# Optimization experiments

Hardware: AMD Instinct MI355X
Metric: run time of the kernel (lower is better)

Reference implementation:

```python
import jax, jax.numpy as jnp
import numpy as np

B, N, C = 2, 2048, 2048
H, KV = 16, 4          # query heads, kv heads
D = C // H             # head_dim = 128
ROPE_BASE = 10000.0


def rope_cos_sin(position_ids, dim):
    # interleaved RoPE: freqs for even indices, repeated pairwise to full dim
    inv_freq = 1.0 / (ROPE_BASE ** (jnp.arange(0, dim, 2, dtype=jnp.float32) / dim))
    ang = position_ids[..., None].astype(jnp.float32) * inv_freq   # [B, N, D/2]
    cos = jnp.repeat(jnp.cos(ang), 2, axis=-1)                     # [B, N, D]
    sin = jnp.repeat(jnp.sin(ang), 2, axis=-1)
    return cos, sin


def rotate_half_interleaved(x):
    # (x0, x1, x2, x3, ...) -> (-x1, x0, -x3, x2, ...)
    x1 = x[..., 0::2]
    x2 = x[..., 1::2]
    return jnp.stack([-x2, x1], axis=-1).reshape(x.shape)


def apply_rotary(x, cos, sin):
    # x: [B, h, N, D]; cos/sin: [B, N, D]
    return x * cos[:, None] + rotate_half_interleaved(x) * sin[:, None]


def setup_inputs() -> dict:
    key = jax.random.key(0)
    ks = jax.random.split(key, 5)
    s = 0.02
    return dict(
        x=jax.random.normal(ks[0], (B, N, C), jnp.float32),
        position_ids=jnp.tile(jnp.arange(N, dtype=jnp.int32), (B, 1)),
        Wq=jax.random.normal(ks[1], (C, C), jnp.float32) * s,
        bq=jnp.zeros((C,), jnp.float32),
        Wk=jax.random.normal(ks[2], (C, KV * D), jnp.float32) * s,
        bk=jnp.zeros((KV * D,), jnp.float32),
        Wv=jax.random.normal(ks[3], (C, KV * D), jnp.float32) * s,
        bv=jnp.zeros((KV * D,), jnp.float32),
        Wo=jax.random.normal(ks[4], (C, C), jnp.float32) * s,
    )


def reference(x, position_ids, Wq, bq, Wk, bk, Wv, bv, Wo):
    Bx, Nx, Cx = x.shape
    q = (x @ Wq + bq).reshape(Bx, Nx, H, D).transpose(0, 2, 1, 3)   # [B,H,N,D]
    k = (x @ Wk + bk).reshape(Bx, Nx, KV, D).transpose(0, 2, 1, 3)  # [B,KV,N,D]
    v = (x @ Wv + bv).reshape(Bx, Nx, KV, D).transpose(0, 2, 1, 3)

    cos, sin = rope_cos_sin(position_ids, D)
    q = apply_rotary(q, cos, sin)
    k = apply_rotary(k, cos, sin)

    # GQA expand: head h uses kv head h // groups (matches unsqueeze+expand+reshape)
    groups = H // KV
    k = jnp.repeat(k, groups, axis=1)   # [B,H,N,D]
    v = jnp.repeat(v, groups, axis=1)

    attn = jnp.einsum('bhqd,bhkd->bhqk', q, k) * (D ** -0.5)        # [B,H,N,N]
    causal_mask = jnp.triu(jnp.ones((Nx, Nx), dtype=bool), 1)
    attn = jnp.where(causal_mask, -jnp.inf, attn)
    attn = jax.nn.softmax(attn, axis=-1)

    out = jnp.einsum('bhqk,bhkd->bhqd', attn, v)
    out = out.transpose(0, 2, 1, 3).reshape(Bx, Nx, Cx)
    return out @ Wo
```

## Files before the change

kernel.cpp:

```cpp
#include <hip/hip_runtime.h>
#include <cstdint>
#include <type_traits>

typedef unsigned short u16;
typedef unsigned int u32;
typedef __bf16 bf16x8 __attribute__((ext_vector_type(8)));
typedef float f32x4 __attribute__((ext_vector_type(4)));

constexpr int BB = 2;
constexpr int SEQ = 2048;
constexpr int CH = 2048;
constexpr int NH = 16;
constexpr int NKV = 4;
constexpr int HD = 128;
constexpr int QKVC = CH + 2 * NKV * HD;

#define DI __device__ __forceinline__

DI u16 f2b(float x) {
  u32 u = __float_as_uint(x);
  u = u + 0x7FFFu + ((u >> 16) & 1u);
  return (u16)(u >> 16);
}
DI float b2f(u16 u) { return __uint_as_float(((u32)u) << 16); }

DI u32 pack2bf(float lo, float hi) {
  return __builtin_amdgcn_perm(__float_as_uint(hi), __float_as_uint(lo), 0x07060302u);
}

DI void glds16(const void* g, void* l) {
  __builtin_amdgcn_global_load_lds(
      (__attribute__((address_space(1))) void*)(uintptr_t)g,
      (__attribute__((address_space(3))) void*)(u32)(uintptr_t)l, 16, 0, 0);
}

__global__ __launch_bounds__(256) void prep_kernel(
    const float* __restrict__ x, u16* __restrict__ xb,
    const float* __restrict__ Wq, const float* __restrict__ Wk,
    const float* __restrict__ Wv, const float* __restrict__ Wo,
    u16* __restrict__ wqkvt, u16* __restrict__ wot) {
  if (blockIdx.z == 4) {
    const int n4 = BB * SEQ * CH / 4;
    int base = (blockIdx.x + 32 * blockIdx.y) * 256 + threadIdx.x;
#pragma unroll
    for (int k = 0; k < 8; k++) {
      int i = base + k * 262144;
      if (i < n4) {
        float4 v = *(const float4*)&x[(size_t)i * 4];
        ushort4 o;
        o.x = f2b(v.x); o.y = f2b(v.y); o.z = f2b(v.z); o.w = f2b(v.w);
        *(ushort4*)&xb[(size_t)i * 4] = o;
      }
    }
    return;
  }
  const int z = blockIdx.z;
  const float* in;
  u16* out;
  int Cc;
  if (z == 0)      { in = Wq; out = wqkvt;                                Cc = CH; }
  else if (z == 1) { in = Wk; out = wqkvt + (size_t)CH * CH;              Cc = NKV * HD; }
  else if (z == 2) { in = Wv; out = wqkvt + (size_t)(CH + NKV * HD) * CH; Cc = NKV * HD; }
  else             { in = Wo; out = wot;                                  Cc = CH; }
  if ((int)blockIdx.y * 64 >= Cc) return;

  __shared__ u16 tile[64 * 65];
  const int r0 = blockIdx.x * 64, c0 = blockIdx.y * 64;
  const int tid = threadIdx.x;
  for (int c = tid; c < 1024; c += 256) {
    int r = c >> 4, col = (c & 15) * 4;
    float4 v = *(const float4*)&in[(size_t)(r0 + r) * Cc + c0 + col];
    tile[r * 65 + col + 0] = f2b(v.x);
    tile[r * 65 + col + 1] = f2b(v.y);
    tile[r * 65 + col + 2] = f2b(v.z);
    tile[r * 65 + col + 3] = f2b(v.w);
  }
  __syncthreads();
  for (int c = tid; c < 1024; c += 256) {
    int r = c >> 4, col = (c & 15) * 4;
    ushort4 v;
    v.x = tile[(col + 0) * 65 + r];
    v.y = tile[(col + 1) * 65 + r];
    v.z = tile[(col + 2) * 65 + r];
    v.w = tile[(col + 3) * 65 + r];
    *(ushort4*)&out[(size_t)(c0 + r) * CH + r0 + col] = v;
  }
}

template <int MODE>
__global__ __launch_bounds__(512, 2) void gemm256_kernel(
    const u16* __restrict__ A, const u16* __restrict__ Bt,
    u16* __restrict__ Cb, float* __restrict__ Cf, u16* __restrict__ Vn,
    const float* __restrict__ bq, const float* __restrict__ bk,
    const float* __restrict__ bv, int M, int Nn, int K) {
  constexpr int BM = 128;
  constexpr int BN = (MODE == 0) ? 384 : 256;
  constexpr int NJ = (MODE == 0) ? 6 : 4;
  extern __shared__ char smem[];
  u16* As = (u16*)smem;
  u16* Bs = As + 2 * BM * 64;

  const int tid = threadIdx.x;
  const int lane = tid & 63, wave = tid >> 6;
  const int wrow = wave >> 2, wcol = wave & 3;
  const int lm = lane & 15, lq = lane >> 4;
  const int m0 = blockIdx.x * BM, n0 = blockIdx.y * BN;
  const int rr = tid >> 3;
  const int sswz8 = ((tid & 7) ^ (rr & 7)) * 8;

  f32x4 acc[4][NJ] = {};

  const int NT = K >> 6;

  if constexpr (MODE == 0) {
    auto stA = [&](int kt, int bsel, int h) {
      glds16(A + (size_t)(m0 + h * 64 + rr) * K + kt + sswz8,
             (char*)As + bsel * (BM * 128) + (h * 64 + wave * 8) * 128);
    };
    auto stB = [&](int kt, int bsel, int q, int s) {
      int g = 96 * ((s * 64 + rr) >> 5) + 32 * q + (rr & 31);
      glds16(Bt + (size_t)(n0 + g) * K + kt + sswz8,
             (char*)Bs + bsel * (BN * 128) + (q * 128 + s * 64 + wave * 8) * 128);
    };

    stA(0, 0, 0); stA(0, 0, 1);
    stB(0, 0, 0, 0); stB(0, 0, 0, 1);
    stB(0, 0, 1, 0); stB(0, 0, 1, 1);
    stB(0, 0, 2, 0); stB(0, 0, 2, 1);
    asm volatile("s_waitcnt vmcnt(0)" ::: "memory");
    __builtin_amdgcn_s_barrier();

    bf16x8 af[4][2];
    for (int T = 0; T < NT; T++) {
      const int buf = T & 1, nb = buf ^ 1;
      const u16* Asb = As + buf * (BM * 64);
      const u16* Bsb = Bs + buf * (BN * 64);
      const int kt1 = (T + 1) << 6;
      const bool pf = (T + 1 < NT);
#pragma unroll
      for (int q = 0; q < 3; q++) {
        if (q == 0) {
#pragma unroll
          for (int ii = 0; ii < 4; ii++)
#pragma unroll
            for (int kk = 0; kk < 2; kk++)
              af[ii][kk] = *(const bf16x8*)&Asb[(wrow * 64 + ii * 16 + lm) * 64 +
                                                ((kk * 4 + lq) ^ (lm & 7)) * 8];
        }
        bf16x8 bfq[2][2];
#pragma unroll
        for (int jj = 0; jj < 2; jj++)
#pragma unroll
          for (int kk = 0; kk < 2; kk++)
            bfq[jj][kk] = *(const bf16x8*)&Bsb[(q * 128 + wcol * 32 + jj * 16 + lm) * 64 +
                                               ((kk * 4 + lq) ^ (lm & 7)) * 8];
        if (pf) {
          if (q == 0) { stA(kt1, nb, 0); stA(kt1, nb, 1); stB(kt1, nb, 0, 0); stB(kt1, nb, 0, 1); }
          else if (q == 1) { stB(kt1, nb, 1, 0); stB(kt1, nb, 1, 1); }
          else { stB(kt1, nb, 2, 0); stB(kt1, nb, 2, 1); }
        }
        __builtin_amdgcn_s_barrier();
        asm volatile("s_waitcnt lgkmcnt(0)" ::: "memory");
        __builtin_amdgcn_sched_barrier(0);
        __builtin_amdgcn_s_setprio(1);
#pragma unroll
        for (int kk = 0; kk < 2; kk++)
#pragma unroll
          for (int ii = 0; ii < 4; ii++)
#pragma unroll
            for (int jj = 0; jj < 2; jj++)
              acc[ii][q * 2 + jj] = __builtin_amdgcn_mfma_f32_16x16x32_bf16(
                  af[ii][kk], bfq[jj][kk], acc[ii][q * 2 + jj], 0, 0, 0);
        __builtin_amdgcn_s_setprio(0);
        if (q == 0) {
          if (pf) asm volatile("s_waitcnt vmcnt(6)" ::: "memory");
          else    asm volatile("s_waitcnt vmcnt(2)" ::: "memory");
        } else if (q == 1) {
          if (pf) asm volatile("s_waitcnt vmcnt(6)" ::: "memory");
          else    asm volatile("s_waitcnt vmcnt(0)" ::: "memory");
        } else if (pf) {
          asm volatile("s_waitcnt vmcnt(4)" ::: "memory");
        }
        __builtin_amdgcn_s_barrier();
      }
    }
  } else {
    auto stageA = [&](int kt, int bsel, int half) {
      const int rb = (wave & 3) * 8 + (wave >> 2) * 64 + half * 32;
      glds16(A + (size_t)(m0 + rb + (lane >> 3)) * K + kt + sswz8,
             (char*)As + bsel * (BM * 128) + rb * 128);
    };
    auto stageB = [&](int kt, int bsel, int half) {
#pragma unroll
      for (int j = 0; j < 2; j++) {
        const int rb = (wave & 3) * 8 + (j * 2 + (wave >> 2)) * 64 + half * 32;
        glds16(Bt + (size_t)(n0 + rb + (lane >> 3)) * K + kt + sswz8,
               (char*)Bs + bsel * 32768 + rb * 128);
      }
    };

    stageA(0, 0, 0); stageB(0, 0, 0); stageB(0, 0, 1); stageA(0, 0, 1);
    asm volatile("s_waitcnt vmcnt(0)" ::: "memory");
    __builtin_amdgcn_s_barrier();

    bf16x8 bf1[4][2];
    for (int T = 0; T < NT; T++) {
      const int buf = T & 1;
      const u16* Asb = As + buf * (BM * 64);
      const u16* Bsb = Bs + buf * (256 * 64);
      const int kt1 = (T + 1) << 6;
      const bool pf = (T + 1 < NT);
      bf16x8 af[2][2];
#pragma unroll
      for (int q = 0; q < 2; q++) {
#pragma unroll
        for (int ii = 0; ii < 2; ii++)
#pragma unroll
          for (int kk = 0; kk < 2; kk++)
            af[ii][kk] = *(const bf16x8*)&Asb[(wrow * 64 + (q * 2 + ii) * 16 + lm) * 64 +
                                              ((kk * 4 + lq) ^ (lm & 7)) * 8];
        if (q == 0) {
#pragma unroll
          for (int j = 0; j < 4; j++)
#pragma unroll
            for (int kk = 0; kk < 2; kk++)
              bf1[j][kk] = *(const bf16x8*)&Bsb[(wcol * 64 + j * 16 + lm) * 64 +
                                                ((kk * 4 + lq) ^ (lm & 7)) * 8];
        }
        if (pf) {
          if (q == 0) { stageA(kt1, buf ^ 1, 0); stageB(kt1, buf ^ 1, 0); stageB(kt1, buf ^ 1, 1); }
          else stageA(kt1, buf ^ 1, 1);
        }
        __builtin_amdgcn_s_barrier();
        asm volatile("s_waitcnt lgkmcnt(0)" ::: "memory");
        __builtin_amdgcn_sched_barrier(0);
        __builtin_amdgcn_s_setprio(1);
#pragma unroll
        for (int kk = 0; kk < 2; kk++)
#pragma unroll
          for (int ii = 0; ii < 2; ii++)
#pragma unroll
            for (int j = 0; j < 4; j++)
              acc[q * 2 + ii][j] = __builtin_amdgcn_mfma_f32_16x16x32_bf16(
                  af[ii][kk], bf1[j][kk], acc[q * 2 + ii][j], 0, 0, 0);
        __builtin_amdgcn_s_setprio(0);
        if (q == 0) {
          if (pf) asm volatile("s_waitcnt vmcnt(5)" ::: "memory");
          else    asm volatile("s_waitcnt vmcnt(0)" ::: "memory");
        } else if (pf) {
          asm volatile("s_waitcnt vmcnt(1)" ::: "memory");
        }
        __builtin_amdgcn_s_barrier();
      }
    }
  }

#pragma unroll
  for (int i = 0; i < 4; i++) {
    const int mg = m0 + wrow * 64 + i * 16 + lq * 4;
#pragma unroll
    for (int j = 0; j < NJ; j++) {
      const int ng = n0 + wcol * (NJ * 16) + j * 16 + lm;
      float bias = 0.f;
      if (MODE == 0)
        bias = (ng < CH) ? bq[ng] : (ng < CH + NKV * HD ? bk[ng - CH] : bv[ng - CH - NKV * HD]);
#pragma unroll
      for (int r = 0; r < 4; r++) {
        float v = acc[i][j][r] + bias;
        if (MODE == 0) {
          if (ng >= CH + NKV * HD) {
            int tok = mg + r;
            int bidx = tok >> 11, n = tok & (SEQ - 1);
            int vcol = ng - (CH + NKV * HD);
            int kh = vcol >> 7, d = vcol & (HD - 1);
            Vn[((size_t)(bidx * NKV + kh) * SEQ + n) * HD + d] = f2b(v);
          } else {
            Cb[(size_t)(mg + r) * Nn + ng] = f2b(v);
          }
        } else {
          Cf[(size_t)(mg + r) * Nn + ng] = v;
        }
      }
    }
  }
}

__global__ __launch_bounds__(256) void ropevt_kernel(
    const u16* __restrict__ qkv, const int* __restrict__ pos,
    u16* __restrict__ Qo, u16* __restrict__ Ko,
    const u16* __restrict__ vin, u16* __restrict__ vout) {
  const int bid = blockIdx.x;
  const int t = threadIdx.x;
  if (bid < BB * SEQ) {
    __shared__ float cs_s[64], sn_s[64];
    const int tok = bid;
    const int b = tok >> 11, n = tok & (SEQ - 1);
    const u16* row = qkv + (size_t)tok * QKVC;
    const float LN1E4_64 = 0.14391156831212788f;

    if (t < 64) {
      float ang = (float)pos[tok] * expf(-(float)t * LN1E4_64);
      float sn, cs;
      sincosf(ang, &sn, &cs);
      cs_s[t] = cs;
      sn_s[t] = sn;
    }
    __syncthreads();

    for (int idx = t; idx < NH * 64; idx += 256) {
      int hh = idx >> 6, i = idx & 63;
      float cs = cs_s[i], sn = sn_s[i];
      float q0v = b2f(row[hh * 128 + 2 * i]);
      float q1v = b2f(row[hh * 128 + 2 * i + 1]);
      size_t off = ((size_t)(b * NH + hh) * SEQ + n) * HD + 2 * i;
      Qo[off] = f2b(q0v * cs - q1v * sn);
      Qo[off + 1] = f2b(q1v * cs + q0v * sn);
    }
    {
      int kh = t >> 6, i = t & 63;
      float cs = cs_s[i], sn = sn_s[i];
      float k0v = b2f(row[CH + kh * 128 + 2 * i]);
      float k1v = b2f(row[CH + kh * 128 + 2 * i + 1]);
      int d0 = 2 * i;
      int g = d0 >> 3;
      int gp = (g & 8) | ((g ^ n) & 7);
      int dp = gp * 8 + (d0 & 7);
      size_t off = ((size_t)(b * NKV + kh) * SEQ + n) * HD + dp;
      Ko[off] = f2b(k0v * cs - k1v * sn);
      Ko[off + 1] = f2b(k1v * cs + k0v * sn);
    }
    return;
  }
  __shared__ u16 tile[64 * 65];
  const int li = bid - BB * SEQ;
  const int n0 = (li & 31) * 64, d0 = ((li >> 5) & 1) * 64, s = li >> 6;
  const u16* ip = vin + (size_t)s * SEQ * HD + (size_t)n0 * HD + d0;
  u16* op = vout + (size_t)s * HD * SEQ + (size_t)d0 * SEQ + n0;
  for (int c = t; c < 1024; c += 256) {
    int r = c >> 4, col = (c & 15) * 4;
    ushort4 v = *(const ushort4*)&ip[(size_t)r * HD + col];
    tile[r * 65 + col + 0] = v.x;
    tile[r * 65 + col + 1] = v.y;
    tile[r * 65 + col + 2] = v.z;
    tile[r * 65 + col + 3] = v.w;
  }
  __syncthreads();
  for (int c = t; c < 1024; c += 256) {
    int r = c >> 4, col = (c & 15) * 4;
    ushort4 v;
    v.x = tile[(col + 0) * 65 + r];
    v.y = tile[(col + 1) * 65 + r];
    v.z = tile[(col + 2) * 65 + r];
    v.w = tile[(col + 3) * 65 + r];
    int u = col;
    int w = (u & 3) | (((u >> 5) & 1) << 2) | (((u >> 2) & 3) << 3) | (((u >> 4) & 1) << 5);
    int glp = (w >> 3) ^ (r & 7);
    int colp = glp * 8 + (w & 7);
    *(ushort4*)&op[(size_t)r * SEQ + colp] = v;
  }
}

__global__ __launch_bounds__(256, 2) void flash_kernel(
    const u16* __restrict__ Q, const u16* __restrict__ Kk,
    const u16* __restrict__ Vt, u16* __restrict__ Oo) {
  __shared__ u16 Kb[2][64 * 128];
  __shared__ u16 Vb[2][144 * 64];
  const int tid = threadIdx.x, lane = tid & 63, wave = tid >> 6;
  const int lm = lane & 15, lq = lane >> 4;
  const int p = blockIdx.x;
  const int h = blockIdx.y, b = blockIdx.z;
  const int q0A = p * 64, q0B = (31 - p) * 64;
  const int kvh = h >> 2;
  const u16* Qg = Q + (size_t)(b * NH + h) * SEQ * HD;
  const u16* Kg = Kk + (size_t)(b * NKV + kvh) * SEQ * HD;
  const u16* Vg = Vt + (size_t)(b * NKV + kvh) * HD * SEQ;

  if (tid < 128) Vb[tid >> 6][128 * 64 + (tid & 63)] = 0x3F80;

  bf16x8 qf[2][4];
#pragma unroll
  for (int qg = 0; qg < 2; qg++) {
    const int q0g = qg ? q0B : q0A;
    const u16* qrow = Qg + (size_t)(q0g + wave * 16 + lm) * HD;
#pragma unroll
    for (int kd = 0; kd < 4; kd++)
      qf[qg][kd] = *(const bf16x8*)&qrow[kd * 32 + lq * 8];
  }

  f32x4 oacc[2][8] = {};
  f32x4 oaccS[2] = {};
  const float SCL2 = 0.12754325f;
  const int nIter = 32 - p;

  auto stage = [&](int kv0, int bufi) {
    const char* kb = (const char*)(Kg + (size_t)kv0 * HD);
    char* kl = (char*)&Kb[bufi][0];
    const char* vbb = (const char*)(Vg + (size_t)kv0);
    char* vl = (char*)&Vb[bufi][0];
#pragma unroll
    for (int c = 0; c < 4; c++) {
      int ch = wave * 4 + c;
      glds16(kb + ch * 1024 + lane * 16, kl + ch * 1024);
      glds16(vbb + (size_t)(ch * 8 + (lane >> 3)) * (SEQ * 2) + (lane & 7) * 16,
             vl + ch * 1024);
    }
  };

  stage(0, 0);

  for (int t = 0; t < nIter; t++) {
    __syncthreads();
    if (t + 1 < nIter) stage((t + 1) * 64, (t + 1) & 1);
    const u16* Ks = &Kb[t & 1][0];
    const u16* Vs = &Vb[t & 1][0];
    const int kv0 = t * 64;
    const bool actA = (t <= p);

    auto run = [&](auto dualc) {
      constexpr bool DUAL = decltype(dualc)::value;
      f32x4 sv[2][4] = {};
#pragma unroll
      for (int nt = 0; nt < 4; nt++)
#pragma unroll
        for (int kd = 0; kd < 4; kd++) {
          int g = kd * 4 + lq;
          int gpp = (g & 8) | ((g ^ lm) & 7);
          bf16x8 kf = *(const bf16x8*)&Ks[(nt * 16 + lm) * 128 + gpp * 8];
          sv[1][nt] = __builtin_amdgcn_mfma_f32_16x16x32_bf16(kf, qf[1][kd], sv[1][nt], 0, 0, 0);
          if constexpr (DUAL)
            sv[0][nt] = __builtin_amdgcn_mfma_f32_16x16x32_bf16(kf, qf[0][kd], sv[0][nt], 0, 0, 0);
        }

      alignas(16) u32 pad[2][2][4];
      auto softmax = [&](int qg, int q0g) {
        const int base = q0g + wave * 16;
        if (kv0 + 63 > base) {
          const int qrow = base + lm;
#pragma unroll
          for (int nt = 0; nt < 4; nt++) {
            float pv[4];
#pragma unroll
            for (int r = 0; r < 4; r++) {
              int kvg = kv0 + nt * 16 + lq * 4 + r;
              float e = exp2f(sv[qg][nt][r] * SCL2);
              pv[r] = (kvg > qrow) ? 0.f : e;
            }
            pad[qg][nt & 1][(nt >> 1) * 2 + 0] = pack2bf(pv[0], pv[1]);
            pad[qg][nt & 1][(nt >> 1) * 2 + 1] = pack2bf(pv[2], pv[3]);
          }
        } else {
#pragma unroll
          for (int nt = 0; nt < 4; nt++) {
            float pv[4];
#pragma unroll
            for (int r = 0; r < 4; r++) pv[r] = exp2f(sv[qg][nt][r] * SCL2);
            pad[qg][nt & 1][(nt >> 1) * 2 + 0] = pack2bf(pv[0], pv[1]);
            pad[qg][nt & 1][(nt >> 1) * 2 + 1] = pack2bf(pv[2], pv[3]);
          }
        }
      };
      softmax(1, q0B);
      if constexpr (DUAL) softmax(0, q0A);

#pragma unroll
      for (int ks = 0; ks < 2; ks++) {
        const int glp = (ks * 4 + lq) ^ (lm & 7);
        const bf16x8 pa1 = *(const bf16x8*)&pad[1][ks][0];
        const bf16x8 pa0 = *(const bf16x8*)&pad[0][ks][0];
#pragma unroll
        for (int dt = 0; dt < 8; dt++) {
          bf16x8 vf = *(const bf16x8*)&Vs[(dt * 16 + lm) * 64 + glp * 8];
          oacc[1][dt] = __builtin_amdgcn_mfma_f32_16x16x32_bf16(pa1, vf, oacc[1][dt], 0, 0, 0);
          if constexpr (DUAL)
            oacc[0][dt] = __builtin_amdgcn_mfma_f32_16x16x32_bf16(pa0, vf, oacc[0][dt], 0, 0, 0);
        }
        bf16x8 vf8 = *(const bf16x8*)&Vs[(128 + lm) * 64 + glp * 8];
        oaccS[1] = __builtin_amdgcn_mfma_f32_16x16x32_bf16(pa1, vf8, oaccS[1], 0, 0, 0);
        if constexpr (DUAL)
          oaccS[0] = __builtin_amdgcn_mfma_f32_16x16x32_bf16(pa0, vf8, oaccS[0], 0, 0, 0);
      }
    };
    if (actA) run(std::integral_constant<bool, true>{});
    else      run(std::integral_constant<bool, false>{});
  }

  u16* orow = Oo + (size_t)b * SEQ * CH + (size_t)h * HD;
#pragma unroll
  for (int qg = 0; qg < 2; qg++) {
    const int q0g = qg ? q0B : q0A;
    float inv[4];
#pragma unroll
    for (int r = 0; r < 4; r++) inv[r] = 1.0f / __shfl(oaccS[qg][r], lq * 16);
    const int qrow_base = q0g + wave * 16 + lq * 4;
#pragma unroll
    for (int dt = 0; dt < 8; dt++)
#pragma unroll
      for (int r = 0; r < 4; r++)
        orow[(size_t)(qrow_base + r) * CH + dt * 16 + lm] = f2b(oacc[qg][dt][r] * inv[r]);
  }
}

extern "C" void kernel_launch(void* const* d_in, const int* in_sizes, int n_in,
                              void* d_out, int out_size, void* d_ws, size_t ws_size,
                              hipStream_t stream) {
  const float* x = (const float*)d_in[0];
  const int* pos = (const int*)d_in[1];
  const float* Wq = (const float*)d_in[2];
  const float* bq = (const float*)d_in[3];
  const float* Wk = (const float*)d_in[4];
  const float* bk = (const float*)d_in[5];
  const float* Wv = (const float*)d_in[6];
  const float* bv = (const float*)d_in[7];
  const float* Wo = (const float*)d_in[8];
  float* out = (float*)d_out;

  char* ws = (char*)d_ws;
  u16* xb = (u16*)ws;    ws += (size_t)BB * SEQ * CH * 2;
  u16* wqkvt = (u16*)ws; ws += (size_t)QKVC * CH * 2;
  u16* wot = (u16*)ws;   ws += (size_t)CH * CH * 2;
  u16* qkv = (u16*)ws;   ws += (size_t)BB * SEQ * QKVC * 2;
  u16* qr = (u16*)ws;    ws += (size_t)BB * NH * SEQ * HD * 2;
  u16* kr = (u16*)ws;    ws += (size_t)BB * NKV * SEQ * HD * 2;
  u16* vn = (u16*)ws;    ws += (size_t)BB * NKV * SEQ * HD * 2;
  u16* vt = (u16*)ws;    ws += (size_t)BB * NKV * SEQ * HD * 2;
  u16* ao = (u16*)ws;    ws += (size_t)BB * SEQ * CH * 2;

  static int attr_done = 0;
  if (!attr_done) {
    hipFuncSetAttribute(reinterpret_cast<const void*>(gemm256_kernel<0>),
                        hipFuncAttributeMaxDynamicSharedMemorySize, 131072);
    hipFuncSetAttribute(reinterpret_cast<const void*>(gemm256_kernel<1>),
                        hipFuncAttributeMaxDynamicSharedMemorySize, 131072);
    attr_done = 1;
  }

  prep_kernel<<<dim3(32, 32, 5), 256, 0, stream>>>(x, xb, Wq, Wk, Wv, Wo, wqkvt, wot);
  gemm256_kernel<0><<<dim3(32, 8), 512, 131072, stream>>>(xb, wqkvt, qkv, (float*)nullptr,
                                                          vn, bq, bk, bv, BB * SEQ, QKVC, CH);
  ropevt_kernel<<<dim3(BB * SEQ + SEQ / 64 * 2 * BB * NKV), 256, 0, stream>>>(
      qkv, pos, qr, kr, vn, vt);
  flash_kernel<<<dim3(16, NH, BB), 256, 0, stream>>>(qr, kr, vt, ao);
  gemm256_kernel<1><<<dim3(32, 8), 512, 98304, stream>>>(ao, wot, (u16*)nullptr, out, nullptr,
                                                         nullptr, nullptr, nullptr, BB * SEQ, CH, CH);
}
```

Baseline: 296.0 us.

## Fuse RoPE and softmax scale into QKV GEMM epilogue, split V transpose kernel

The QKV projection GEMM epilogue now applies rotary embedding directly. It uses a per-block cos/sin table built in shared memory and pairs adjacent columns with lane shuffles, then writes rotated Q and swizzled K straight to their attention layouts. This removes the intermediate qkv buffer and the separate RoPE pass over it. The softmax scale is folded into Q before bf16 rounding, which changes numerics slightly. V transposition moves to a small standalone kernel, and the epilogue gains sincos work on every block.

```diff
diff --git a/kernel.cpp b/kernel.cpp
--- a/kernel.cpp
+++ b/kernel.cpp
@@ -87,12 +87,45 @@
   }
 }
 
+__global__ __launch_bounds__(256) void vtrans_kernel(const u16* __restrict__ in,
+                                                     u16* __restrict__ out) {
+  __shared__ u16 tile[64 * 65];
+  const int s = blockIdx.z, n0 = blockIdx.x * 64, d0 = blockIdx.y * 64;
+  const int tid = threadIdx.x;
+  const u16* ip = in + (size_t)s * SEQ * HD + (size_t)n0 * HD + d0;
+  u16* op = out + (size_t)s * HD * SEQ + (size_t)d0 * SEQ + n0;
+  for (int c = tid; c < 1024; c += 256) {
+    int r = c >> 4, col = (c & 15) * 4;
+    ushort4 v = *(const ushort4*)&ip[(size_t)r * HD + col];
+    tile[r * 65 + col + 0] = v.x;
+    tile[r * 65 + col + 1] = v.y;
+    tile[r * 65 + col + 2] = v.z;
+    tile[r * 65 + col + 3] = v.w;
+  }
+  __syncthreads();
+  for (int c = tid; c < 1024; c += 256) {
+    int r = c >> 4, col = (c & 15) * 4;
+    ushort4 v;
+    v.x = tile[(col + 0) * 65 + r];
+    v.y = tile[(col + 1) * 65 + r];
+    v.z = tile[(col + 2) * 65 + r];
+    v.w = tile[(col + 3) * 65 + r];
+    int u = col;
+    int w = (u & 3) | (((u >> 5) & 1) << 2) | (((u >> 2) & 3) << 3) | (((u >> 4) & 1) << 5);
+    int glp = (w >> 3) ^ (r & 7);
+    int colp = glp * 8 + (w & 7);
+    *(ushort4*)&op[(size_t)r * SEQ + colp] = v;
+  }
+}
+
 template <int MODE>
 __global__ __launch_bounds__(512, 2) void gemm256_kernel(
     const u16* __restrict__ A, const u16* __restrict__ Bt,
-    u16* __restrict__ Cb, float* __restrict__ Cf, u16* __restrict__ Vn,
+    u16* __restrict__ Qo, u16* __restrict__ Ko,
+    float* __restrict__ Cf, u16* __restrict__ Vn,
     const float* __restrict__ bq, const float* __restrict__ bk,
-    const float* __restrict__ bv, int M, int Nn, int K) {
+    const float* __restrict__ bv, const int* __restrict__ pos,
+    int M, int Nn, int K) {
   constexpr int BM = 128;
   constexpr int BN = (MODE == 0) ? 384 : 256;
   constexpr int NJ = (MODE == 0) ? 6 : 4;
@@ -255,108 +288,76 @@
     }
   }
 
-#pragma unroll
-  for (int i = 0; i < 4; i++) {
-    const int mg = m0 + wrow * 64 + i * 16 + lq * 4;
-#pragma unroll
-    for (int j = 0; j < NJ; j++) {
-      const int ng = n0 + wcol * (NJ * 16) + j * 16 + lm;
-      float bias = 0.f;
-      if (MODE == 0)
-        bias = (ng < CH) ? bq[ng] : (ng < CH + NKV * HD ? bk[ng - CH] : bv[ng - CH - NKV * HD]);
-#pragma unroll
-      for (int r = 0; r < 4; r++) {
-        float v = acc[i][j][r] + bias;
-        if (MODE == 0) {
-          if (ng >= CH + NKV * HD) {
-            int tok = mg + r;
-            int bidx = tok >> 11, n = tok & (SEQ - 1);
-            int vcol = ng - (CH + NKV * HD);
-            int kh = vcol >> 7, d = vcol & (HD - 1);
-            Vn[((size_t)(bidx * NKV + kh) * SEQ + n) * HD + d] = f2b(v);
-          } else {
-            Cb[(size_t)(mg + r) * Nn + ng] = f2b(v);
+  if constexpr (MODE == 0) {
+    __syncthreads();
+    float2* tab = (float2*)smem;
+    const float LN1E4_64 = 0.14391156831212788f;
+    for (int e = tid; e < 128 * 64; e += 512) {
+      int tk = e >> 6, ii = e & 63;
+      float ang = (float)pos[m0 + tk] * expf(-(float)ii * LN1E4_64);
+      float sn, cs;
+      sincosf(ang, &sn, &cs);
+      tab[e] = make_float2(cs, sn);
+    }
+    __syncthreads();
+    const float SCL2G = 0.12754325f;
+
+#pragma unroll
+    for (int i = 0; i < 4; i++) {
+      const int mg = m0 + wrow * 64 + i * 16 + lq * 4;
+#pragma unroll
+      for (int j = 0; j < NJ; j++) {
+        const int ng = n0 + wcol * 96 + j * 16 + lm;
+        const int reg7 = (n0 + wcol * 96 + j * 16) >> 7;
+        float bias = (ng < CH) ? bq[ng]
+                               : (ng < CH + NKV * HD ? bk[ng - CH] : bv[ng - CH - NKV * HD]);
+        if (reg7 < 16) {
+          const int d = ng & 127, ii = d >> 1, hh = ng >> 7;
+#pragma unroll
+          for (int r = 0; r < 4; r++) {
+            float v = acc[i][j][r] + bias;
+            float vp = __shfl_xor(v, 1);
+            float2 cw = tab[(mg + r - m0) * 64 + ii];
+            float c = cw.x * SCL2G, s = cw.y * SCL2G;
+            float o = fmaf(v, c, (lane & 1) ? vp * s : -(vp * s));
+            int tok = mg + r, bb2 = tok >> 11, n = tok & (SEQ - 1);
+            Qo[((size_t)(bb2 * NH + hh) * SEQ + n) * HD + d] = f2b(o);
+          }
+        } else if (reg7 < 20) {
+          const int d = ng & 127, ii = d >> 1, kh = (ng >> 7) - 16, g = d >> 3;
+#pragma unroll
+          for (int r = 0; r < 4; r++) {
+            float v = acc[i][j][r] + bias;
+            float vp = __shfl_xor(v, 1);
+            float2 cw = tab[(mg + r - m0) * 64 + ii];
+            float o = fmaf(v, cw.x, (lane & 1) ? vp * cw.y : -(vp * cw.y));
+            int tok = mg + r, bb2 = tok >> 11, n = tok & (SEQ - 1);
+            int gp = (g & 8) | ((g ^ n) & 7);
+            Ko[((size_t)(bb2 * NKV + kh) * SEQ + n) * HD + gp * 8 + (d & 7)] = f2b(o);
           }
         } else {
-          Cf[(size_t)(mg + r) * Nn + ng] = v;
-        }
-      }
-    }
-  }
-}
-
-__global__ __launch_bounds__(256) void ropevt_kernel(
-    const u16* __restrict__ qkv, const int* __restrict__ pos,
-    u16* __restrict__ Qo, u16* __restrict__ Ko,
-    const u16* __restrict__ vin, u16* __restrict__ vout) {
-  const int bid = blockIdx.x;
-  const int t = threadIdx.x;
-  if (bid < BB * SEQ) {
-    __shared__ float cs_s[64], sn_s[64];
-    const int tok = bid;
-    const int b = tok >> 11, n = tok & (SEQ - 1);
-    const u16* row = qkv + (size_t)tok * QKVC;
-    const float LN1E4_64 = 0.14391156831212788f;
-
-    if (t < 64) {
-      float ang = (float)pos[tok] * expf(-(float)t * LN1E4_64);
-      float sn, cs;
-      sincosf(ang, &sn, &cs);
-      cs_s[t] = cs;
-      sn_s[t] = sn;
-    }
-    __syncthreads();
-
-    for (int idx = t; idx < NH * 64; idx += 256) {
-      int hh = idx >> 6, i = idx & 63;
-      float cs = cs_s[i], sn = sn_s[i];
-      float q0v = b2f(row[hh * 128 + 2 * i]);
-      float q1v = b2f(row[hh * 128 + 2 * i + 1]);
-      size_t off = ((size_t)(b * NH + hh) * SEQ + n) * HD + 2 * i;
-      Qo[off] = f2b(q0v * cs - q1v * sn);
-      Qo[off + 1] = f2b(q1v * cs + q0v * sn);
-    }
-    {
-      int kh = t >> 6, i = t & 63;
-      float cs = cs_s[i], sn = sn_s[i];
-      float k0v = b2f(row[CH + kh * 128 + 2 * i]);
-      float k1v = b2f(row[CH + kh * 128 + 2 * i + 1]);
-      int d0 = 2 * i;
-      int g = d0 >> 3;
-      int gp = (g & 8) | ((g ^ n) & 7);
-      int dp = gp * 8 + (d0 & 7);
-      size_t off = ((size_t)(b * NKV + kh) * SEQ + n) * HD + dp;
-      Ko[off] = f2b(k0v * cs - k1v * sn);
-      Ko[off + 1] = f2b(k1v * cs + k0v * sn);
-    }
-    return;
-  }
-  __shared__ u16 tile[64 * 65];
-  const int li = bid - BB * SEQ;
-  const int n0 = (li & 31) * 64, d0 = ((li >> 5) & 1) * 64, s = li >> 6;
-  const u16* ip = vin + (size_t)s * SEQ * HD + (size_t)n0 * HD + d0;
-  u16* op = vout + (size_t)s * HD * SEQ + (size_t)d0 * SEQ + n0;
-  for (int c = t; c < 1024; c += 256) {
-    int r = c >> 4, col = (c & 15) * 4;
-    ushort4 v = *(const ushort4*)&ip[(size_t)r * HD + col];
-    tile[r * 65 + col + 0] = v.x;
-    tile[r * 65 + col + 1] = v.y;
-    tile[r * 65 + col + 2] = v.z;
-    tile[r * 65 + col + 3] = v.w;
-  }
-  __syncthreads();
-  for (int c = t; c < 1024; c += 256) {
-    int r = c >> 4, col = (c & 15) * 4;
-    ushort4 v;
-    v.x = tile[(col + 0) * 65 + r];
-    v.y = tile[(col + 1) * 65 + r];
-    v.z = tile[(col + 2) * 65 + r];
-    v.w = tile[(col + 3) * 65 + r];
-    int u = col;
-    int w = (u & 3) | (((u >> 5) & 1) << 2) | (((u >> 2) & 3) << 3) | (((u >> 4) & 1) << 5);
-    int glp = (w >> 3) ^ (r & 7);
-    int colp = glp * 8 + (w & 7);
-    *(ushort4*)&op[(size_t)r * SEQ + colp] = v;
+          const int vcol = ng - (CH + NKV * HD), kh = vcol >> 7, d = vcol & (HD - 1);
+#pragma unroll
+          for (int r = 0; r < 4; r++) {
+            float v = acc[i][j][r] + bias;
+            int tok = mg + r, bb2 = tok >> 11, n = tok & (SEQ - 1);
+            Vn[((size_t)(bb2 * NKV + kh) * SEQ + n) * HD + d] = f2b(v);
+          }
+        }
+      }
+    }
+  } else {
+#pragma unroll
+    for (int i = 0; i < 4; i++) {
+      const int mg = m0 + wrow * 64 + i * 16 + lq * 4;
+#pragma unroll
+      for (int j = 0; j < NJ; j++) {
+        const int ng = n0 + wcol * (NJ * 16) + j * 16 + lm;
+#pragma unroll
+        for (int r = 0; r < 4; r++)
+          Cf[(size_t)(mg + r) * Nn + ng] = acc[i][j][r];
+      }
+    }
   }
 }
 
@@ -389,7 +390,6 @@
 
   f32x4 oacc[2][8] = {};
   f32x4 oaccS[2] = {};
-  const float SCL2 = 0.12754325f;
   const int nIter = 32 - p;
 
   auto stage = [&](int kv0, int bufi) {
@@ -442,7 +442,7 @@
 #pragma unroll
             for (int r = 0; r < 4; r++) {
               int kvg = kv0 + nt * 16 + lq * 4 + r;
-              float e = exp2f(sv[qg][nt][r] * SCL2);
+              float e = exp2f(sv[qg][nt][r]);
               pv[r] = (kvg > qrow) ? 0.f : e;
             }
             pad[qg][nt & 1][(nt >> 1) * 2 + 0] = pack2bf(pv[0], pv[1]);
@@ -453,7 +453,7 @@
           for (int nt = 0; nt < 4; nt++) {
             float pv[4];
 #pragma unroll
-            for (int r = 0; r < 4; r++) pv[r] = exp2f(sv[qg][nt][r] * SCL2);
+            for (int r = 0; r < 4; r++) pv[r] = exp2f(sv[qg][nt][r]);
             pad[qg][nt & 1][(nt >> 1) * 2 + 0] = pack2bf(pv[0], pv[1]);
             pad[qg][nt & 1][(nt >> 1) * 2 + 1] = pack2bf(pv[2], pv[3]);
           }
@@ -518,7 +518,6 @@
   u16* xb = (u16*)ws;    ws += (size_t)BB * SEQ * CH * 2;
   u16* wqkvt = (u16*)ws; ws += (size_t)QKVC * CH * 2;
   u16* wot = (u16*)ws;   ws += (size_t)CH * CH * 2;
-  u16* qkv = (u16*)ws;   ws += (size_t)BB * SEQ * QKVC * 2;
   u16* qr = (u16*)ws;    ws += (size_t)BB * NH * SEQ * HD * 2;
   u16* kr = (u16*)ws;    ws += (size_t)BB * NKV * SEQ * HD * 2;
   u16* vn = (u16*)ws;    ws += (size_t)BB * NKV * SEQ * HD * 2;
@@ -535,11 +534,11 @@
   }
 
   prep_kernel<<<dim3(32, 32, 5), 256, 0, stream>>>(x, xb, Wq, Wk, Wv, Wo, wqkvt, wot);
-  gemm256_kernel<0><<<dim3(32, 8), 512, 131072, stream>>>(xb, wqkvt, qkv, (float*)nullptr,
-                                                          vn, bq, bk, bv, BB * SEQ, QKVC, CH);
-  ropevt_kernel<<<dim3(BB * SEQ + SEQ / 64 * 2 * BB * NKV), 256, 0, stream>>>(
-      qkv, pos, qr, kr, vn, vt);
+  gemm256_kernel<0><<<dim3(32, 8), 512, 131072, stream>>>(
+      xb, wqkvt, qr, kr, (float*)nullptr, vn, bq, bk, bv, pos, BB * SEQ, QKVC, CH);
+  vtrans_kernel<<<dim3(SEQ / 64, HD / 64, BB * NKV), 256, 0, stream>>>(vn, vt);
   flash_kernel<<<dim3(16, NH, BB), 256, 0, stream>>>(qr, kr, vt, ao);
-  gemm256_kernel<1><<<dim3(32, 8), 512, 98304, stream>>>(ao, wot, (u16*)nullptr, out, nullptr,
-                                                         nullptr, nullptr, nullptr, BB * SEQ, CH, CH);
-}
+  gemm256_kernel<1><<<dim3(32, 8), 512, 98304, stream>>>(
+      ao, wot, nullptr, nullptr, out, nullptr, nullptr, nullptr, nullptr, nullptr,
+      BB * SEQ, CH, CH);
+}
```

New measurement: 287.2 us. 3.0% less time.
